# Performance work log

Measured on AMD Instinct MI355X. Metric: run time of the kernel, lower is better.

## Reference

```python
import jax, jax.numpy as jnp
import numpy as np

TEMPERATURE = 0.07
EPS = 1e-12  # F.normalize eps


def _l2norm(x):
    n = jnp.linalg.norm(x, axis=-1, keepdims=True)
    return x / jnp.maximum(n, EPS)


def setup_inputs() -> dict:
    key = jax.random.key(0)
    k1, k2 = jax.random.split(key)
    B, T, H = 16, 512, 1024
    h_source = jax.random.normal(k1, (B, T, H), dtype=jnp.float32)
    h_target = jax.random.normal(k2, (B, T, H), dtype=jnp.float32)
    src_mask = jnp.ones((B, T), dtype=bool)
    tgt_mask = jnp.ones((B, T), dtype=bool)
    return {"h_source": h_source, "h_target": h_target,
            "src_mask": src_mask, "tgt_mask": tgt_mask}


def reference(h_source, h_target, src_mask, tgt_mask):
    # Masks are all-True and B*T == max_samples, so boolean selection == reshape
    # and the random subsampling branch is never taken (deterministic path).
    H = h_source.shape[-1]
    h_s = h_source.reshape(-1, H).astype(jnp.float32)          # (N, H)
    h_t = jax.lax.stop_gradient(h_target.reshape(-1, H)).astype(jnp.float32)  # detached

    h_s_norm = _l2norm(h_s)                                     # (N, H)
    h_t_norm = _l2norm(h_t)                                     # (M, H)
    sim = h_s_norm @ h_t_norm.T                                 # (N, M) cosine sim

    pos_idx = jnp.argmax(sim, axis=1)                           # == topk_idx[:, 0]
    logits = sim / TEMPERATURE
    # cross-entropy with pos_idx labels (stable log-softmax)
    logp = jax.nn.log_softmax(logits, axis=1)
    l_contrastive = -jnp.mean(jnp.take_along_axis(logp, pos_idx[:, None], axis=1)[:, 0])

    # contextual consistency: adjacent source tokens' NN embeddings should align
    nn_embeds = h_t_norm[pos_idx]                               # (N, H)
    nn_sim = jnp.sum(nn_embeds[:-1] * nn_embeds[1:], axis=-1)   # (N-1,)
    l_contextual = 1.0 - jnp.mean(nn_sim)

    return (l_contrastive, l_contextual)
```

## Files before the change

### kernel.cpp

```cpp
#include <hip/hip_runtime.h>
#include <hip/hip_bf16.h>
#include <stdint.h>


#define HDIM 1024
#define NROW 8192
#define TEMP_INV (1.0f / 0.07f)

typedef __attribute__((ext_vector_type(4))) float float4v;
typedef __attribute__((ext_vector_type(2))) float float2v;
typedef __attribute__((ext_vector_type(4))) int   int4v;
typedef __attribute__((ext_vector_type(8))) int   int8v;

#define SN_OFF   ((size_t)0)
#define TN_OFF   ((size_t)8388608)
#define TR_OFF   ((size_t)16777216)
#define SUM_OFF  ((size_t)25165824)
#define PMX_OFF  (SUM_OFF + 32768)
#define ACC_OFF  (PMX_OFF + 65536)
#define CNT_OFF  (ACC_OFF + 64)

static __device__ __forceinline__ void gload_lds16(const void* gptr, void* lptr) {
    __builtin_amdgcn_global_load_lds(
        (const __attribute__((address_space(1))) void*)gptr,
        (__attribute__((address_space(3))) void*)(uintptr_t)(uint32_t)(uintptr_t)lptr,
        16, 0, 0);
}

static __device__ __forceinline__ float fp8dot4(unsigned a, unsigned b) {
    float2v al = __builtin_amdgcn_cvt_pk_f32_fp8((int)a, false);
    float2v ah = __builtin_amdgcn_cvt_pk_f32_fp8((int)a, true);
    float2v bl = __builtin_amdgcn_cvt_pk_f32_fp8((int)b, false);
    float2v bh = __builtin_amdgcn_cvt_pk_f32_fp8((int)b, true);
    return al[0]*bl[0] + al[1]*bl[1] + ah[0]*bh[0] + ah[1]*bh[1];
}

__global__ __launch_bounds__(256)
void norm_kernel(const float* __restrict__ hs, const float* __restrict__ ht,
                 char* __restrict__ Sn, char* __restrict__ Tn, char* __restrict__ Tr,
                 float* __restrict__ sumexp, unsigned long long* __restrict__ pmax,
                 float* __restrict__ acc, unsigned* __restrict__ cnt) {
    const int b = blockIdx.x;
    const int t = threadIdx.x;
    const int wave = t >> 6, lane = t & 63;
    const bool isT = (b >= 512);
    const int g = isT ? (b - 512) : b;
    const float* in = (isT ? ht : hs) + (size_t)g * 16 * HDIM;
    char* outTiled = (isT ? Tn : Sn) + (size_t)g * 16384;

    __shared__ float sq[16][256];
    __shared__ float sscale[16];

    float4v v[16];
    #pragma unroll
    for (int i = 0; i < 16; ++i) {
        v[i] = ((const float4v*)in)[i * 256 + t];
        sq[i][t] = v[i][0]*v[i][0] + v[i][1]*v[i][1] + v[i][2]*v[i][2] + v[i][3]*v[i][3];
    }
    __syncthreads();
    #pragma unroll
    for (int j = 0; j < 4; ++j) {
        const int ri = wave * 4 + j;
        float s = sq[ri][lane] + sq[ri][lane + 64] + sq[ri][lane + 128] + sq[ri][lane + 192];
        #pragma unroll
        for (int off = 1; off < 64; off <<= 1) s += __shfl_xor(s, off);
        if (lane == 0) sscale[ri] = 1.0f / fmaxf(sqrtf(s), 1e-12f);
    }
    __syncthreads();

    char* tiled = (char*)sq;
    const int koff = (t >> 5) * 2048 + ((t >> 2) & 1) * 1024
                   + ((t >> 3) & 3) * 256 + (t & 3) * 4;
    #pragma unroll
    for (int i = 0; i < 16; ++i) {
        const float sc = sscale[i];
        int d = __builtin_amdgcn_cvt_pk_fp8_f32(v[i][0]*sc, v[i][1]*sc, 0, false);
        d     = __builtin_amdgcn_cvt_pk_fp8_f32(v[i][2]*sc, v[i][3]*sc, d, true);
        *(int*)(tiled + koff + i * 16) = d;
        if (isT) ((int*)(Tr + (size_t)(g * 16 + i) * HDIM))[t] = d;
    }
    __syncthreads();
    #pragma unroll
    for (int j = 0; j < 4; ++j)
        ((uint4*)outTiled)[j * 256 + t] = ((const uint4*)tiled)[j * 256 + t];

    if (!isT && t < 16) { sumexp[b * 16 + t] = 0.f; pmax[b * 16 + t] = 0ull; }
    if (b == 0 && t == 16) { acc[0] = 0.f; acc[1] = 0.f; *cnt = 0u; }
}

__global__ __launch_bounds__(256)
__attribute__((amdgpu_waves_per_eu(3, 3)))
void flash_kernel(const char* __restrict__ Sn, const char* __restrict__ Tn,
                  float* __restrict__ sumexp, unsigned long long* __restrict__ pmax) {
    __shared__ __align__(16) char As[16384];
    __shared__ __align__(16) char Bs[16384];
    const int t = threadIdx.x;
    const int wave = t >> 6, lane = t & 63;
    const int quad = lane >> 4, l16 = lane & 15;
    const int rbase = (int)(blockIdx.x & 63) * 128;
    const int cbase = (int)(blockIdx.x >> 6) * 128;
    const int wr = wave & 1, wc = wave >> 1;
    const int wm = wr * 64, wn = wc * 64;

    int offA[4], offB[4];
    #pragma unroll
    for (int u = 0; u < 4; ++u) {
        int ua = wave * 4 + u;
        offA[u] = (rbase / 16 + (ua >> 1)) * 16384 + (ua & 1) * 1024 + lane * 16;
        offB[u] = (cbase / 16 + (ua >> 1)) * 16384 + (ua & 1) * 1024 + lane * 16;
    }

    float4v acc[4][4];
    #pragma unroll
    for (int i = 0; i < 4; ++i)
        #pragma unroll
        for (int j = 0; j < 4; ++j) acc[i][j] = (float4v){0.f, 0.f, 0.f, 0.f};
    const int usc = 0x7f7f7f7f;

    const int aBase = wr * 4 * 2048 + lane * 16;
    const int bBase = wc * 4 * 2048 + lane * 16;

    #pragma unroll 1
    for (int kb = 0; kb < 8; ++kb) {
        const int ks = kb * 2048;
        #pragma unroll
        for (int u = 0; u < 4; ++u)
            gload_lds16(Sn + offA[u] + ks, As + (wave * 4 + u) * 1024);
        #pragma unroll
        for (int u = 0; u < 4; ++u)
            gload_lds16(Tn + offB[u] + ks, Bs + (wave * 4 + u) * 1024);
        asm volatile("s_waitcnt vmcnt(0)\ns_barrier" ::: "memory");

        int8v af[4];
        #pragma unroll
        for (int i = 0; i < 4; ++i) {
            int4v lo = *(const int4v*)(As + aBase + i * 2048);
            int4v hi = *(const int4v*)(As + aBase + i * 2048 + 1024);
            af[i] = __builtin_shufflevector(lo, hi, 0, 1, 2, 3, 4, 5, 6, 7);
        }
        __builtin_amdgcn_s_setprio(1);
        #pragma unroll
        for (int j = 0; j < 4; ++j) {
            int4v lo = *(const int4v*)(Bs + bBase + j * 2048);
            int4v hi = *(const int4v*)(Bs + bBase + j * 2048 + 1024);
            int8v bf = __builtin_shufflevector(lo, hi, 0, 1, 2, 3, 4, 5, 6, 7);
            #pragma unroll
            for (int i = 0; i < 4; ++i)
                acc[i][j] = __builtin_amdgcn_mfma_scale_f32_16x16x128_f8f6f4(
                    af[i], bf, acc[i][j], 0, 0, 0, usc, 0, usc);
        }
        __builtin_amdgcn_s_setprio(0);
        __syncthreads();
    }

    float se_v[4][4]; unsigned long long pk_v[4][4];
    #pragma unroll
    for (int i = 0; i < 4; ++i) {
        #pragma unroll
        for (int r = 0; r < 4; ++r) {
            float se = 0.f; float mx = -2.f; int mi = 0x7fffffff;
            #pragma unroll
            for (int j = 0; j < 4; ++j) {
                float v = acc[i][j][r];
                se += __expf(v * TEMP_INV);
                int col = cbase + wn + j * 16 + l16;
                if (v > mx || (v == mx && col < mi)) { mx = v; mi = col; }
            }
            #pragma unroll
            for (int off = 1; off < 16; off <<= 1) {
                se += __shfl_xor(se, off);
                float om = __shfl_xor(mx, off);
                int oi = __shfl_xor(mi, off);
                if (om > mx || (om == mx && oi < mi)) { mx = om; mi = oi; }
            }
            se_v[i][r] = se;
            pk_v[i][r] = ((unsigned long long)__float_as_uint(mx + 2.0f) << 32)
                         | (unsigned long long)(0xffffffffu - (unsigned)mi);
        }
    }
    float* pbSe = (float*)Bs;
    unsigned long long* pbPk = (unsigned long long*)(Bs + 512);
    if (wave < 2 && l16 == 0) {
        #pragma unroll
        for (int i = 0; i < 4; ++i)
            #pragma unroll
            for (int r = 0; r < 4; ++r) {
                int rl = wm + i * 16 + quad * 4 + r;
                pbSe[rl] = se_v[i][r]; pbPk[rl] = pk_v[i][r];
            }
    }
    __syncthreads();
    if (wave >= 2 && l16 == 0) {
        #pragma unroll
        for (int i = 0; i < 4; ++i)
            #pragma unroll
            for (int r = 0; r < 4; ++r) {
                int rl = wm + i * 16 + quad * 4 + r;
                float se = se_v[i][r] + pbSe[rl];
                unsigned long long pk = pk_v[i][r];
                unsigned long long po = pbPk[rl];
                if (po > pk) pk = po;
                atomicAdd(&sumexp[rbase + rl], se);
                atomicMax(&pmax[rbase + rl], pk);
            }
    }
}

__global__ __launch_bounds__(256)
void tail_kernel(const float* __restrict__ sumexp,
                 const unsigned long long* __restrict__ pmax,
                 const char* __restrict__ Tr,
                 float* __restrict__ acc, unsigned* __restrict__ cnt,
                 float* __restrict__ out) {
    const int blk = blockIdx.x;
    const int t = threadIdx.x, wave = t >> 6, lane = t & 63;

    if (wave == 0) {
        int r = blk * 32 + (lane & 31);
        unsigned long long p = pmax[r];
        float mx = __uint_as_float((unsigned)(p >> 32)) - 2.0f;
        float loss = logf(sumexp[r]) - mx * TEMP_INV;
        #pragma unroll
        for (int off = 1; off < 32; off <<= 1) loss += __shfl_xor(loss, off);
        if (lane == 0) atomicAdd(acc + 0, loss);
    }

    float s = 0.f;
    #pragma unroll
    for (int it = 0; it < 8; ++it) {
        int g = blk * 32 + wave * 8 + it;
        if (g < NROW - 1) {
            unsigned long long pa = pmax[g], pb = pmax[g + 1];
            int ia = (int)(0xffffffffu - (unsigned)(pa & 0xffffffffu));
            int ib = (int)(0xffffffffu - (unsigned)(pb & 0xffffffffu));
            uint4 va = ((const uint4*)(Tr + (size_t)ia * HDIM))[lane];
            uint4 vb = ((const uint4*)(Tr + (size_t)ib * HDIM))[lane];
            s += fp8dot4(va.x, vb.x) + fp8dot4(va.y, vb.y)
               + fp8dot4(va.z, vb.z) + fp8dot4(va.w, vb.w);
        }
    }
    #pragma unroll
    for (int off = 1; off < 64; off <<= 1) s += __shfl_xor(s, off);
    __shared__ float red[4];
    if (lane == 0) red[wave] = s;
    __syncthreads();
    if (t == 0) atomicAdd(acc + 1, red[0] + red[1] + red[2] + red[3]);

    __threadfence();
    __shared__ unsigned done;
    if (t == 0) done = atomicAdd(cnt, 1u);
    __syncthreads();
    if (t == 0 && done == 255u) {
        float l0 = atomicAdd(acc + 0, 0.0f);
        float l1 = atomicAdd(acc + 1, 0.0f);
        out[0] = l0 / (float)NROW;
        out[1] = 1.0f - l1 / (float)(NROW - 1);
    }
}

extern "C" void kernel_launch(void* const* d_in, const int* in_sizes, int n_in,
                              void* d_out, int out_size, void* d_ws, size_t ws_size,
                              hipStream_t stream) {
    const float* hs = (const float*)d_in[0];
    const float* ht = (const float*)d_in[1];
    char* ws = (char*)d_ws;
    char* Sn = ws + SN_OFF;
    char* Tn = ws + TN_OFF;
    char* Tr = ws + TR_OFF;
    float* sumexp = (float*)(ws + SUM_OFF);
    unsigned long long* pmax = (unsigned long long*)(ws + PMX_OFF);
    float* acc = (float*)(ws + ACC_OFF);
    unsigned* cnt = (unsigned*)(ws + CNT_OFF);
    float* out = (float*)d_out;

    norm_kernel<<<1024, 256, 0, stream>>>(hs, ht, Sn, Tn, Tr, sumexp, pmax, acc, cnt);
    flash_kernel<<<4096, 256, 0, stream>>>(Sn, Tn, sumexp, pmax);
    tail_kernel<<<256, 256, 0, stream>>>(sumexp, pmax, Tr, acc, cnt, out);
}
```

Before: 247.8 us.

## Raise flash kernel occupancy, swizzle blocks across XCDs, and stream the epilogue reduction

The block-to-tile mapping is remapped so that each XCD (bid&7) handles a fixed group of column tiles and neighbouring blocks share row and column tiles, aiming for better L2 reuse. The waves-per-EU hint goes from 3 to 4. To fit the lower register budget, the epilogue now reduces one i-slice at a time with barriers in between instead of holding all 16 partial results. A union replaces the shufflevector for fragment assembly. The higher occupancy risks register spills, and the per-slice epilogue adds extra barriers.

```diff
diff --git a/kernel.cpp b/kernel.cpp
--- a/kernel.cpp
+++ b/kernel.cpp
@@ -89,7 +89,7 @@
 }
 
 __global__ __launch_bounds__(256)
-__attribute__((amdgpu_waves_per_eu(3, 3)))
+__attribute__((amdgpu_waves_per_eu(4, 4)))
 void flash_kernel(const char* __restrict__ Sn, const char* __restrict__ Tn,
                   float* __restrict__ sumexp, unsigned long long* __restrict__ pmax) {
     __shared__ __align__(16) char As[16384];
@@ -97,8 +97,15 @@
     const int t = threadIdx.x;
     const int wave = t >> 6, lane = t & 63;
     const int quad = lane >> 4, l16 = lane & 15;
-    const int rbase = (int)(blockIdx.x & 63) * 128;
-    const int cbase = (int)(blockIdx.x >> 6) * 128;
+
+    const int bid = (int)blockIdx.x;
+    const int xcd = bid & 7;
+    const int idx = bid >> 3;
+    const int oct = idx >> 6;
+    const int w   = idx & 63;
+    const int rbase = (oct * 8 + (w & 7)) * 128;
+    const int cbase = (xcd * 8 + (w >> 3)) * 128;
+
     const int wr = wave & 1, wc = wave >> 1;
     const int wm = wr * 64, wn = wc * 64;
 
@@ -120,6 +127,8 @@
     const int aBase = wr * 4 * 2048 + lane * 16;
     const int bBase = wc * 4 * 2048 + lane * 16;
 
+    union fragu { int8v v8; int4v v4[2]; };
+
     #pragma unroll 1
     for (int kb = 0; kb < 8; ++kb) {
         const int ks = kb * 2048;
@@ -131,31 +140,32 @@
             gload_lds16(Tn + offB[u] + ks, Bs + (wave * 4 + u) * 1024);
         asm volatile("s_waitcnt vmcnt(0)\ns_barrier" ::: "memory");
 
-        int8v af[4];
+        fragu af[4];
         #pragma unroll
         for (int i = 0; i < 4; ++i) {
-            int4v lo = *(const int4v*)(As + aBase + i * 2048);
-            int4v hi = *(const int4v*)(As + aBase + i * 2048 + 1024);
-            af[i] = __builtin_shufflevector(lo, hi, 0, 1, 2, 3, 4, 5, 6, 7);
+            af[i].v4[0] = *(const int4v*)(As + aBase + i * 2048);
+            af[i].v4[1] = *(const int4v*)(As + aBase + i * 2048 + 1024);
         }
         __builtin_amdgcn_s_setprio(1);
         #pragma unroll
         for (int j = 0; j < 4; ++j) {
-            int4v lo = *(const int4v*)(Bs + bBase + j * 2048);
-            int4v hi = *(const int4v*)(Bs + bBase + j * 2048 + 1024);
-            int8v bf = __builtin_shufflevector(lo, hi, 0, 1, 2, 3, 4, 5, 6, 7);
+            fragu bf;
+            bf.v4[0] = *(const int4v*)(Bs + bBase + j * 2048);
+            bf.v4[1] = *(const int4v*)(Bs + bBase + j * 2048 + 1024);
             #pragma unroll
             for (int i = 0; i < 4; ++i)
                 acc[i][j] = __builtin_amdgcn_mfma_scale_f32_16x16x128_f8f6f4(
-                    af[i], bf, acc[i][j], 0, 0, 0, usc, 0, usc);
+                    af[i].v8, bf.v8, acc[i][j], 0, 0, 0, usc, 0, usc);
         }
         __builtin_amdgcn_s_setprio(0);
         __syncthreads();
     }
 
-    float se_v[4][4]; unsigned long long pk_v[4][4];
-    #pragma unroll
+    float* pbSe = (float*)Bs;
+    unsigned long long* pbPk = (unsigned long long*)(Bs + 512);
+    #pragma unroll 1
     for (int i = 0; i < 4; ++i) {
+        float se_r[4]; unsigned long long pk_r[4];
         #pragma unroll
         for (int r = 0; r < 4; ++r) {
             float se = 0.f; float mx = -2.f; int mi = 0x7fffffff;
@@ -173,36 +183,31 @@
                 int oi = __shfl_xor(mi, off);
                 if (om > mx || (om == mx && oi < mi)) { mx = om; mi = oi; }
             }
-            se_v[i][r] = se;
-            pk_v[i][r] = ((unsigned long long)__float_as_uint(mx + 2.0f) << 32)
-                         | (unsigned long long)(0xffffffffu - (unsigned)mi);
-        }
-    }
-    float* pbSe = (float*)Bs;
-    unsigned long long* pbPk = (unsigned long long*)(Bs + 512);
-    if (wave < 2 && l16 == 0) {
-        #pragma unroll
-        for (int i = 0; i < 4; ++i)
+            se_r[r] = se;
+            pk_r[r] = ((unsigned long long)__float_as_uint(mx + 2.0f) << 32)
+                      | (unsigned long long)(0xffffffffu - (unsigned)mi);
+        }
+        if (wave < 2 && l16 == 0) {
             #pragma unroll
             for (int r = 0; r < 4; ++r) {
                 int rl = wm + i * 16 + quad * 4 + r;
-                pbSe[rl] = se_v[i][r]; pbPk[rl] = pk_v[i][r];
-            }
-    }
-    __syncthreads();
-    if (wave >= 2 && l16 == 0) {
-        #pragma unroll
-        for (int i = 0; i < 4; ++i)
+                pbSe[rl] = se_r[r]; pbPk[rl] = pk_r[r];
+            }
+        }
+        __syncthreads();
+        if (wave >= 2 && l16 == 0) {
             #pragma unroll
             for (int r = 0; r < 4; ++r) {
                 int rl = wm + i * 16 + quad * 4 + r;
-                float se = se_v[i][r] + pbSe[rl];
-                unsigned long long pk = pk_v[i][r];
+                float se = se_r[r] + pbSe[rl];
+                unsigned long long pk = pk_r[r];
                 unsigned long long po = pbPk[rl];
                 if (po > pk) pk = po;
                 atomicAdd(&sumexp[rbase + rl], se);
                 atomicMax(&pmax[rbase + rl], pk);
             }
+        }
+        __syncthreads();
     }
 }
 
```

New measurement: 524.0 us. 111% more time.
